# Optimization experiments

Measured on AMD Instinct MI355X. Metric: run time of the kernel, lower is better.

The kernel has to match this reference:

```python
import jax, jax.numpy as jnp
import numpy as np

LN_EPS = 1e-5


def _act_quant(x):
    # per-token int8 absmax quantization (BitNet style)
    s = 127.0 / jnp.clip(jnp.max(jnp.abs(x), axis=-1, keepdims=True), 1e-5)
    return jnp.clip(jnp.round(x * s), -128.0, 127.0) / s


def _weight_quant(w):
    # ternary 1.58-bit weight quantization with global mean-abs scale
    s = 1.0 / jnp.clip(jnp.mean(jnp.abs(w)), 1e-5)
    return jnp.clip(jnp.round(w * s), -1.0, 1.0) / s


def _ste(x, q):
    # straight-through estimator: forward uses q, gradient flows through x
    return x + jax.lax.stop_gradient(q - x)


def _bitlinear(x, w, b):
    xq = _ste(x, _act_quant(x))
    wq = _ste(w, _weight_quant(w))
    return jnp.einsum('bsd,hd->bsh', xq, wq) + b


def _layernorm(x, gamma, beta):
    mu = jnp.mean(x, axis=-1, keepdims=True)
    var = jnp.mean(jnp.square(x - mu), axis=-1, keepdims=True)
    return (x - mu) * jax.lax.rsqrt(var + LN_EPS) * gamma + beta


def setup_inputs() -> dict:
    key = jax.random.key(0)
    ks = jax.random.split(key, 3)
    B, S, D, H = 4, 4096, 2048, 8192
    return {
        'x': jax.random.normal(ks[0], (B, S, D), dtype=jnp.float32),
        'gamma': jnp.ones((D,), jnp.float32),
        'beta': jnp.zeros((D,), jnp.float32),
        'w1': jax.random.normal(ks[1], (H, D), jnp.float32) * (1.0 / np.sqrt(D)),
        'b1': jnp.zeros((H,), jnp.float32),
        'w2': jax.random.normal(ks[2], (D, H), jnp.float32) * (1.0 / np.sqrt(H)),
        'b2': jnp.zeros((D,), jnp.float32),
    }


def reference(x, gamma, beta, w1, b1, w2, b2):
    h = _layernorm(x, gamma, beta)
    h = _bitlinear(h, w1, b1)            # [B,S,H]
    h = jax.nn.gelu(h, approximate=False)  # torch nn.GELU default = exact erf
    out = _bitlinear(h, w2, b2)          # [B,S,D]
    return out
```

## Files before the change

### kernel.cpp

```cpp
#include <hip/hip_runtime.h>
#include <hip/hip_bf16.h>


typedef __attribute__((ext_vector_type(4))) int int4v;

#define D_DIM 2048
#define H_DIM 8192
#define M_DIM 16384
#define MCHUNK 4096

__device__ __forceinline__ float block_sum(float v, float* buf) {
#pragma unroll
  for (int o = 32; o > 0; o >>= 1) v += __shfl_down(v, o, 64);
  const int lane = threadIdx.x & 63, w = threadIdx.x >> 6;
  if (lane == 0) buf[w] = v;
  __syncthreads();
  float r = buf[0] + buf[1] + buf[2] + buf[3];
  __syncthreads();
  return r;
}
__device__ __forceinline__ float block_max(float v, float* buf) {
#pragma unroll
  for (int o = 32; o > 0; o >>= 1) v = fmaxf(v, __shfl_down(v, o, 64));
  const int lane = threadIdx.x & 63, w = threadIdx.x >> 6;
  if (lane == 0) buf[w] = v;
  __syncthreads();
  float r = fmaxf(fmaxf(buf[0], buf[1]), fmaxf(buf[2], buf[3]));
  __syncthreads();
  return r;
}

__device__ __forceinline__ void lds16(const signed char* g, signed char* l) {
  __builtin_amdgcn_global_load_lds(
      (const __attribute__((address_space(1))) unsigned int*)g,
      (__attribute__((address_space(3))) unsigned int*)l, 16, 0, 0);
}

__global__ __launch_bounds__(256) void absmean_partial2(const float* __restrict__ w1,
                                                        const float* __restrict__ w2,
                                                        int n, double* __restrict__ part1,
                                                        double* __restrict__ part2) {
  __shared__ float buf[4];
  const int half = gridDim.x >> 1;
  const bool second = (int)blockIdx.x >= half;
  const float* w = second ? w2 : w1;
  double* part = second ? part2 : part1;
  const int bid = second ? (blockIdx.x - half) : blockIdx.x;
  float s = 0.0f;
  const long stride = (long)half * 256 * 4;
  for (long i = ((long)bid * 256 + threadIdx.x) * 4; i < n; i += stride) {
    float4 v = *(const float4*)(w + i);
    s += fabsf(v.x) + fabsf(v.y) + fabsf(v.z) + fabsf(v.w);
  }
  float r = block_sum(s, buf);
  if (threadIdx.x == 0) part[bid] = (double)r;
}

__global__ __launch_bounds__(256) void absmean_final2(const double* __restrict__ part1,
                                                      const double* __restrict__ part2,
                                                      int nb, double n,
                                                      double* __restrict__ out) {
  __shared__ double buf[4];
  const double* part = (blockIdx.x == 0) ? part1 : part2;
  double s = 0.0;
  for (int i = threadIdx.x; i < nb; i += 256) s += part[i];
#pragma unroll
  for (int o = 32; o > 0; o >>= 1) s += __shfl_down(s, o, 64);
  const int lane = threadIdx.x & 63, w = threadIdx.x >> 6;
  if (lane == 0) buf[w] = s;
  __syncthreads();
  if (threadIdx.x == 0) out[blockIdx.x] = (buf[0] + buf[1] + buf[2] + buf[3]) / n;
}

__global__ __launch_bounds__(256) void wquant2_kernel(const float* __restrict__ w1,
                                                      const float* __restrict__ w2,
                                                      const double* __restrict__ means,
                                                      signed char* __restrict__ wq1,
                                                      signed char* __restrict__ wq2, int n) {
  const int half = gridDim.x >> 1;
  const bool second = (int)blockIdx.x >= half;
  const float* w = second ? w2 : w1;
  signed char* wq = second ? wq2 : wq1;
  const double mean = second ? means[1] : means[0];
  const int bid = second ? (blockIdx.x - half) : blockIdx.x;
  long i = ((long)bid * 256 + threadIdx.x) * 4;
  if (i >= n) return;
  const float s = 1.0f / (float)fmax(mean, 1e-5);
  float4 v = *(const float4*)(w + i);
  __align__(4) signed char q[4];
  q[0] = (signed char)(int)fminf(fmaxf(rintf(v.x * s), -1.f), 1.f);
  q[1] = (signed char)(int)fminf(fmaxf(rintf(v.y * s), -1.f), 1.f);
  q[2] = (signed char)(int)fminf(fmaxf(rintf(v.z * s), -1.f), 1.f);
  q[3] = (signed char)(int)fminf(fmaxf(rintf(v.w * s), -1.f), 1.f);
  *(int*)(wq + i) = *(int*)q;
}

__global__ __launch_bounds__(256) void ln_quant_kernel(const float* __restrict__ x,
                                                       const float* __restrict__ gamma,
                                                       const float* __restrict__ beta,
                                                       signed char* __restrict__ aq,
                                                       float* __restrict__ ds) {
  __shared__ float buf[4];
  const int t = threadIdx.x;
  const long row = blockIdx.x;
  const float* xr = x + row * (long)D_DIM;
  float v[8];
  *(float4*)(v)     = *(const float4*)(xr + t * 8);
  *(float4*)(v + 4) = *(const float4*)(xr + t * 8 + 4);
  float s = 0.f;
#pragma unroll
  for (int i = 0; i < 8; ++i) s += v[i];
  s = block_sum(s, buf);
  const float mu = s * (1.0f / 2048.0f);
  float sq = 0.f;
#pragma unroll
  for (int i = 0; i < 8; ++i) { float d = v[i] - mu; sq += d * d; }
  sq = block_sum(sq, buf);
  const float inv = 1.0f / sqrtf(sq * (1.0f / 2048.0f) + 1e-5f);
  float gam[8], bet[8];
  *(float4*)(gam)     = *(const float4*)(gamma + t * 8);
  *(float4*)(gam + 4) = *(const float4*)(gamma + t * 8 + 4);
  *(float4*)(bet)     = *(const float4*)(beta + t * 8);
  *(float4*)(bet + 4) = *(const float4*)(beta + t * 8 + 4);
  float xn[8]; float am = 0.f;
#pragma unroll
  for (int i = 0; i < 8; ++i) {
    xn[i] = (v[i] - mu) * inv * gam[i] + bet[i];
    am = fmaxf(am, fabsf(xn[i]));
  }
  am = block_max(am, buf);
  am = fmaxf(am, 1e-5f);
  const float qs = 127.0f / am;
  __align__(8) signed char q[8];
#pragma unroll
  for (int i = 0; i < 8; ++i)
    q[i] = (signed char)(int)fminf(fmaxf(rintf(xn[i] * qs), -128.f), 127.f);
  *(long*)(aq + row * D_DIM + t * 8) = *(long*)q;
  if (t == 0) ds[row] = am / 127.0f;
}

__global__ __launch_bounds__(256) void hquant32_kernel(const float* __restrict__ src,
                                                       signed char* __restrict__ dst,
                                                       float* __restrict__ ds2) {
  __shared__ float buf[4];
  const int t = threadIdx.x;
  const long row = blockIdx.x;
  const float* sr = src + row * (long)H_DIM;
  float v[4][8];
#pragma unroll
  for (int c = 0; c < 4; ++c) {
    *(float4*)(v[c])     = *(const float4*)(sr + (c * 256 + t) * 8);
    *(float4*)(v[c] + 4) = *(const float4*)(sr + (c * 256 + t) * 8 + 4);
  }
  float am = 0.f;
#pragma unroll
  for (int c = 0; c < 4; ++c)
#pragma unroll
    for (int i = 0; i < 8; ++i) am = fmaxf(am, fabsf(v[c][i]));
  am = block_max(am, buf);
  am = fmaxf(am, 1e-5f);
  const float qs = 127.0f / am;
  signed char* dr = dst + row * (long)H_DIM;
#pragma unroll
  for (int c = 0; c < 4; ++c) {
    __align__(8) signed char o[8];
#pragma unroll
    for (int i = 0; i < 8; ++i)
      o[i] = (signed char)(int)fminf(fmaxf(rintf(v[c][i] * qs), -128.f), 127.f);
    *(long*)(dr + (c * 256 + t) * 8) = *(long*)o;
  }
  if (t == 0) ds2[row] = am / 127.0f;
}

__device__ __forceinline__ void read_a2(const signed char* sm, int base, int4v (&af)[2]) {
#pragma unroll
  for (int ms = 0; ms < 2; ++ms)
    af[ms] = *(const int4v*)&sm[base + ms * 1024];
}
__device__ __forceinline__ void read_b4(const signed char* sm, int base, int4v (&bf)[4]) {
#pragma unroll
  for (int ns = 0; ns < 4; ++ns)
    bf[ns] = *(const int4v*)&sm[base + ns * 1024];
}
__device__ __forceinline__ void mfma_half(const int4v (&af)[2], const int4v (&bf)[4],
                                          int4v (&acc)[4][4], int m0) {
#pragma unroll
  for (int ms = 0; ms < 2; ++ms)
#pragma unroll
    for (int ns = 0; ns < 4; ++ns)
      acc[m0 + ms][ns] = __builtin_amdgcn_mfma_i32_16x16x64_i8(
          af[ms], bf[ns], acc[m0 + ms][ns], 0, 0, 0);
}

template <int EPI>
__global__ __launch_bounds__(512, 4) void gemm256_kernel(
    const signed char* __restrict__ A,
    const signed char* __restrict__ Bm,
    const float* __restrict__ dsA,
    const double* __restrict__ meanw,
    const float* __restrict__ bias,
    float* __restrict__ outf,
    int NBX, int N, int K) {
  __shared__ __align__(16) signed char smA[2 * 256 * 64];
  __shared__ __align__(16) signed char smB[2 * 128 * 64];
  const int tid = threadIdx.x;
  const int lane = tid & 63;
  const int wid = tid >> 6;
  const int wr = wid >> 1;
  const int wcn = wid & 1;

  const int cpx = gridDim.x >> 3;
  const int swz = ((int)blockIdx.x & 7) * cpx + ((int)blockIdx.x >> 3);
  const int bx = swz % NBX, by = swz / NBX;
  const long r0 = (long)by * 256;
  const long c0 = (long)bx * 128;

  const int srow = tid >> 2;
  const int schunk = (tid & 3) ^ (srow & 3) ^ ((srow >> 2) & 3);
  const signed char* gAs = A + (r0 + srow) * (long)K + schunk * 16;
  const signed char* gBs = Bm + (c0 + srow) * (long)K + schunk * 16;

  const int frow = lane & 15;
  const int fchunk = (lane >> 4) ^ (frow & 3) ^ ((frow >> 2) & 3);
  const int fbyte = frow * 64 + fchunk * 16;
  const int baseA = (wr >> 1) * 8192 + (wr & 1) * 4096 + fbyte;
  const int baseB = wcn * 4096 + fbyte;

  int4v acc[4][4] = {};
  int4v af[2], bf[4];
  const int nk = K >> 6;
  const int nk2 = nk >> 1;

#define STGA(h, t, d)                                                         \
    lds16(gAs + (long)((h) * 128) * K + (long)(t) * 64,                       \
          &smA[(d) * 16384 + (h) * 8192 + tid * 16]);
#define STGB(t, d)                                                            \
    lds16(gBs + (long)(t) * 64, &smB[(d) * 8192 + tid * 16]);
#define BAR  __builtin_amdgcn_s_barrier()
#define SCB  __builtin_amdgcn_sched_barrier(0)
#define LGKM0 asm volatile("s_waitcnt lgkmcnt(0)" ::: "memory")
#define PRIO1 __builtin_amdgcn_s_setprio(1)
#define PRIO0 __builtin_amdgcn_s_setprio(0)

  STGA(0, 0, 0); STGA(1, 0, 0); STGB(0, 0);
  STGB(1, 1);
  asm volatile("s_waitcnt vmcnt(1)" ::: "memory");
  SCB; BAR; SCB;

  for (int i = 0; i < nk2; ++i) {
    const int t0 = 2 * i, t1 = 2 * i + 1;
    const bool s = (i < nk2 - 1);

    read_a2(smA, baseA, af);
    read_b4(smB, baseB, bf);
    STGA(0, t1, 1); STGA(1, t1, 1);
    SCB; BAR; LGKM0; SCB;
    PRIO1; mfma_half(af, bf, acc, 0); PRIO0;
    SCB; BAR;

    read_a2(smA, baseA + 2048, af);
    if (s) STGB(t0 + 2, 0);
    SCB; BAR; LGKM0; SCB;
    PRIO1; mfma_half(af, bf, acc, 2); PRIO0;
    SCB;
    if (s) { asm volatile("s_waitcnt vmcnt(1)" ::: "memory"); }
    else   { asm volatile("s_waitcnt vmcnt(0)" ::: "memory"); }
    SCB; BAR;

    read_a2(smA, 16384 + baseA, af);
    read_b4(smB, 8192 + baseB, bf);
    if (s) { STGA(0, t0 + 2, 0); STGA(1, t0 + 2, 0); }
    SCB; BAR; LGKM0; SCB;
    PRIO1; mfma_half(af, bf, acc, 0); PRIO0;
    SCB; BAR;

    read_a2(smA, 16384 + baseA + 2048, af);
    if (s) STGB(t1 + 2, 1);
    SCB; BAR; LGKM0; SCB;
    PRIO1; mfma_half(af, bf, acc, 2); PRIO0;
    SCB;
    if (s) { asm volatile("s_waitcnt vmcnt(1)" ::: "memory"); }
    else   { asm volatile("s_waitcnt vmcnt(0)" ::: "memory"); }
    SCB; BAR;
  }
#undef STGA
#undef STGB
#undef BAR
#undef SCB
#undef LGKM0
#undef PRIO1
#undef PRIO0

  const float sw = (float)fmax(meanw[0], 1e-5);
#pragma unroll
  for (int m = 0; m < 4; ++m) {
#pragma unroll
    for (int j = 0; j < 4; ++j) {
      const long row = r0 + wr * 64 + m * 16 + (lane >> 4) * 4 + j;
      const float sa = dsA[row] * sw;
#pragma unroll
      for (int n = 0; n < 4; ++n) {
        const long col = c0 + wcn * 64 + n * 16 + (lane & 15);
        float v = (float)acc[m][n][j] * sa + bias[col];
        if (EPI == 1) {
          float gl = 0.5f * v * (1.0f + erff(v * 0.70710678118654752f));
          outf[row * (long)N + col] = gl;
        } else {
          outf[row * (long)N + col] = v;
        }
      }
    }
  }
}

extern "C" void kernel_launch(void* const* d_in, const int* in_sizes, int n_in,
                              void* d_out, int out_size, void* d_ws, size_t ws_size,
                              hipStream_t stream) {
  const float* x     = (const float*)d_in[0];
  const float* gamma = (const float*)d_in[1];
  const float* beta  = (const float*)d_in[2];
  const float* w1    = (const float*)d_in[3];
  const float* b1    = (const float*)d_in[4];
  const float* w2    = (const float*)d_in[5];
  const float* b2    = (const float*)d_in[6];

  char* ws = (char*)d_ws;
  double* part1 = (double*)(ws + 0);
  double* part2 = (double*)(ws + 16384);
  double* means = (double*)(ws + 32768);
  float* ds1  = (float*)(ws + 65536);
  float* ds2  = (float*)(ws + 131072);
  signed char* wq1 = (signed char*)(ws + 1048576l);
  signed char* wq2 = (signed char*)(ws + 17825792l);
  signed char* aq  = (signed char*)(ws + 34603008l);
  signed char* hq  = (signed char*)(ws + 68157440l);

  const int NW = 16777216;
  float* hstage = (float*)d_out;

  absmean_partial2<<<4096, 256, 0, stream>>>(w1, w2, NW, part1, part2);
  absmean_final2<<<2, 256, 0, stream>>>(part1, part2, 2048, (double)NW, means);
  wquant2_kernel<<<32768, 256, 0, stream>>>(w1, w2, means, wq1, wq2, NW);
  ln_quant_kernel<<<16384, 256, 0, stream>>>(x, gamma, beta, aq, ds1);

  for (int c = 0; c < 4; ++c) {
    const long r0 = (long)c * MCHUNK;
    gemm256_kernel<1><<<(H_DIM / 128) * (MCHUNK / 256), 512, 0, stream>>>(
        aq + r0 * D_DIM, wq1, ds1 + r0, means + 0, b1, hstage,
        H_DIM / 128, H_DIM, D_DIM);
    hquant32_kernel<<<MCHUNK, 256, 0, stream>>>(
        hstage, hq + r0 * H_DIM, ds2 + r0);
  }

  gemm256_kernel<2><<<(D_DIM / 128) * (M_DIM / 256), 512, 0, stream>>>(
      hq, wq2, ds2, means + 1, b2, (float*)d_out,
      D_DIM / 128, D_DIM, H_DIM);
}
```

Measured before the change: 875.7 us.

## Triple-buffer A tiles in LDS to prefetch two K-steps ahead

The int8 GEMM's LDS staging changes from double buffering with a two-iteration unrolled loop to a three-slot ring for A and rotating offsets for B. A tiles are now loaded two K-steps ahead, and the vmcnt waits change to allow more loads in flight. This aims to hide global-load latency better, at the cost of more LDS per block (which may reduce occupancy at 4 blocks/CU) and runtime offset rotation in place of constant offsets.

New measurement: 883.2 us. Within noise of the previous version (+0.9%).

```diff
diff --git a/kernel.cpp b/kernel.cpp
--- a/kernel.cpp
+++ b/kernel.cpp
@@ -182,8 +182,8 @@
   for (int ns = 0; ns < 4; ++ns)
     bf[ns] = *(const int4v*)&sm[base + ns * 1024];
 }
-__device__ __forceinline__ void mfma_half(const int4v (&af)[2], const int4v (&bf)[4],
-                                          int4v (&acc)[4][4], int m0) {
+__device__ __forceinline__ void mfma_half16(const int4v (&af)[2], const int4v (&bf)[4],
+                                            int4v (&acc)[4][4], int m0) {
 #pragma unroll
   for (int ms = 0; ms < 2; ++ms)
 #pragma unroll
@@ -201,7 +201,7 @@
     const float* __restrict__ bias,
     float* __restrict__ outf,
     int NBX, int N, int K) {
-  __shared__ __align__(16) signed char smA[2 * 256 * 64];
+  __shared__ __align__(16) signed char smA[3 * 256 * 64];
   __shared__ __align__(16) signed char smB[2 * 128 * 64];
   const int tid = threadIdx.x;
   const int lane = tid & 63;
@@ -229,13 +229,12 @@
   int4v acc[4][4] = {};
   int4v af[2], bf[4];
   const int nk = K >> 6;
-  const int nk2 = nk >> 1;
-
-#define STGA(h, t, d)                                                         \
+
+#define STGA(h, t, off)                                                       \
     lds16(gAs + (long)((h) * 128) * K + (long)(t) * 64,                       \
-          &smA[(d) * 16384 + (h) * 8192 + tid * 16]);
-#define STGB(t, d)                                                            \
-    lds16(gBs + (long)(t) * 64, &smB[(d) * 8192 + tid * 16]);
+          &smA[(off) + (h) * 8192 + tid * 16]);
+#define STGB(t, off)                                                          \
+    lds16(gBs + (long)(t) * 64, &smB[(off) + tid * 16]);
 #define BAR  __builtin_amdgcn_s_barrier()
 #define SCB  __builtin_amdgcn_sched_barrier(0)
 #define LGKM0 asm volatile("s_waitcnt lgkmcnt(0)" ::: "memory")
@@ -243,45 +242,34 @@
 #define PRIO0 __builtin_amdgcn_s_setprio(0)
 
   STGA(0, 0, 0); STGA(1, 0, 0); STGB(0, 0);
-  STGB(1, 1);
-  asm volatile("s_waitcnt vmcnt(1)" ::: "memory");
+  STGA(0, 1, 16384); STGA(1, 1, 16384); STGB(1, 8192);
+  asm volatile("s_waitcnt vmcnt(3)" ::: "memory");
   SCB; BAR; SCB;
 
-  for (int i = 0; i < nk2; ++i) {
-    const int t0 = 2 * i, t1 = 2 * i + 1;
-    const bool s = (i < nk2 - 1);
-
-    read_a2(smA, baseA, af);
-    read_b4(smB, baseB, bf);
-    STGA(0, t1, 1); STGA(1, t1, 1);
+  int aC = 0, aN = 16384, aN2 = 32768;
+  int bC = 0;
+
+  for (int t = 0; t < nk; ++t) {
+    const bool s = (t + 2 < nk);
+
+    read_a2(smA, aC + baseA, af);
+    read_b4(smB, bC + baseB, bf);
+    if (s) { STGA(0, t + 2, aN2); STGA(1, t + 2, aN2); }
     SCB; BAR; LGKM0; SCB;
-    PRIO1; mfma_half(af, bf, acc, 0); PRIO0;
+    PRIO1; mfma_half16(af, bf, acc, 0); PRIO0;
     SCB; BAR;
 
-    read_a2(smA, baseA + 2048, af);
-    if (s) STGB(t0 + 2, 0);
+    read_a2(smA, aC + baseA + 2048, af);
+    if (s) STGB(t + 2, bC);
     SCB; BAR; LGKM0; SCB;
-    PRIO1; mfma_half(af, bf, acc, 2); PRIO0;
+    PRIO1; mfma_half16(af, bf, acc, 2); PRIO0;
     SCB;
-    if (s) { asm volatile("s_waitcnt vmcnt(1)" ::: "memory"); }
+    if (s) { asm volatile("s_waitcnt vmcnt(3)" ::: "memory"); }
     else   { asm volatile("s_waitcnt vmcnt(0)" ::: "memory"); }
     SCB; BAR;
 
-    read_a2(smA, 16384 + baseA, af);
-    read_b4(smB, 8192 + baseB, bf);
-    if (s) { STGA(0, t0 + 2, 0); STGA(1, t0 + 2, 0); }
-    SCB; BAR; LGKM0; SCB;
-    PRIO1; mfma_half(af, bf, acc, 0); PRIO0;
-    SCB; BAR;
-
-    read_a2(smA, 16384 + baseA + 2048, af);
-    if (s) STGB(t1 + 2, 1);
-    SCB; BAR; LGKM0; SCB;
-    PRIO1; mfma_half(af, bf, acc, 2); PRIO0;
-    SCB;
-    if (s) { asm volatile("s_waitcnt vmcnt(1)" ::: "memory"); }
-    else   { asm volatile("s_waitcnt vmcnt(0)" ::: "memory"); }
-    SCB; BAR;
+    const int tmp = aC; aC = aN; aN = aN2; aN2 = tmp;
+    bC ^= 8192;
   }
 #undef STGA
 #undef STGB
```
